# Optimization experiments

Hardware: AMD Instinct MI355X
Metric: run time of the kernel (lower is better)

## Reference

```python
import jax, jax.numpy as jnp
import numpy as np

B, F, U = 32768, 32, 256


def setup_inputs() -> dict:
    key = jax.random.key(0)
    k1, k2, k3 = jax.random.split(key, 3)
    inputs = jax.random.normal(k1, (B, F), dtype=jnp.float32)
    # weight sampled near 1 so the F-way product stays finite in fp32
    weight = 1.0 + 0.1 * jax.random.normal(k2, (F, U), dtype=jnp.float32)
    weight_selector = jax.random.normal(k3, (F, U), dtype=jnp.float32)
    bias = jnp.zeros((U,), dtype=jnp.float32)
    return {"inputs": inputs, "weight": weight,
            "weight_selector": weight_selector, "bias": bias}


def reference(inputs, weight, weight_selector, bias):
    # Faithful to CustomNeuron.call: the tf.map_fn(custom_function, ...) result
    # is dead code (immediately overwritten), so the output is
    #   prod_f( inputs[b,f] * weight[f,u] ) + bias[u]   -> [B, U]
    expand_matrix = inputs[:, :, None] * weight[None, :, :]  # [B, F, U]
    return jnp.prod(expand_matrix, axis=1) + bias  # [B, U]
```

## Files before the change

kernel.cpp:

```cpp
#include <hip/hip_runtime.h>


#define F 32
#define U 256
#define ROWS_PER_BLOCK 32

__global__ __launch_bounds__(256)
void custom_neuron_kernel(const float* __restrict__ inp,
                          const float* __restrict__ weight,
                          const float* __restrict__ bias,
                          float* __restrict__ out) {
  __shared__ float pin_s[ROWS_PER_BLOCK];
  const int tid = threadIdx.x;
  const int base = blockIdx.x * ROWS_PER_BLOCK;

  const int c = (tid & 63) * 4;
  float4 w = make_float4(1.f, 1.f, 1.f, 1.f);
#pragma unroll
  for (int f = 0; f < F; ++f) {
    const float4 wf = *(const float4*)(weight + f * U + c);
    w.x *= wf.x; w.y *= wf.y; w.z *= wf.z; w.w *= wf.w;
  }
  const float4 b = *(const float4*)(bias + c);

  {
    const float4 x = *(const float4*)(inp + (size_t)base * F + tid * 4);
    float p = x.x * x.y * x.z * x.w;
    p *= __shfl_xor(p, 1);
    p *= __shfl_xor(p, 2);
    p *= __shfl_xor(p, 4);
    if ((tid & 7) == 0) pin_s[tid >> 3] = p;
  }
  __syncthreads();

  const int r0 = tid >> 6;
#pragma unroll
  for (int k = 0; k < 8; ++k) {
    const int row = r0 + 4 * k;
    const float p = pin_s[row];
    float4 o;
    o.x = p * w.x + b.x;
    o.y = p * w.y + b.y;
    o.z = p * w.z + b.z;
    o.w = p * w.w + b.w;
    *(float4*)(out + (size_t)(base + row) * U + c) = o;
  }
}

extern "C" void kernel_launch(void* const* d_in, const int* in_sizes, int n_in,
                              void* d_out, int out_size, void* d_ws, size_t ws_size,
                              hipStream_t stream) {
  const float* inp    = (const float*)d_in[0];
  const float* weight = (const float*)d_in[1];
  const float* bias   = (const float*)d_in[3];
  float* out = (float*)d_out;

  const int B = in_sizes[0] / F;
  const int grid = B / ROWS_PER_BLOCK;
  custom_neuron_kernel<<<grid, 256, 0, stream>>>(inp, weight, bias, out);
}
```

Before: 74.67 us.

## Precompute weight column products in a separate kernel and use one row per wave

New measurement: 75.58 us. No clear change (+1.2%).

```diff
diff --git a/kernel.cpp b/kernel.cpp
--- a/kernel.cpp
+++ b/kernel.cpp
@@ -3,48 +3,44 @@
 
 #define F 32
 #define U 256
-#define ROWS_PER_BLOCK 32
+#define B_TOTAL 32768
 
 __global__ __launch_bounds__(256)
-void custom_neuron_kernel(const float* __restrict__ inp,
-                          const float* __restrict__ weight,
-                          const float* __restrict__ bias,
-                          float* __restrict__ out) {
-  __shared__ float pin_s[ROWS_PER_BLOCK];
-  const int tid = threadIdx.x;
-  const int base = blockIdx.x * ROWS_PER_BLOCK;
+void pw_kernel(const float* __restrict__ weight, float* __restrict__ pw) {
+  const int u = threadIdx.x;
+  float p = 1.0f;
+#pragma unroll
+  for (int f = 0; f < F; ++f) p *= weight[f * U + u];
+  pw[u] = p;
+}
 
-  const int c = (tid & 63) * 4;
-  float4 w = make_float4(1.f, 1.f, 1.f, 1.f);
-#pragma unroll
-  for (int f = 0; f < F; ++f) {
-    const float4 wf = *(const float4*)(weight + f * U + c);
-    w.x *= wf.x; w.y *= wf.y; w.z *= wf.z; w.w *= wf.w;
+__global__ __launch_bounds__(256)
+void main_kernel(const float* __restrict__ inp, const float* __restrict__ pw,
+                 const float* __restrict__ bias, float* __restrict__ out) {
+  const int lane = threadIdx.x & 63;
+  const int wave = threadIdx.x >> 6;
+  const int row = blockIdx.x * 4 + wave;
+
+  float p = 1.0f;
+  if (lane < 8) {
+    const float4 x = *(const float4*)(inp + (size_t)row * F + lane * 4);
+    p = x.x * x.y * x.z * x.w;
   }
-  const float4 b = *(const float4*)(bias + c);
+  p *= __shfl_xor(p, 1);
+  p *= __shfl_xor(p, 2);
+  p *= __shfl_xor(p, 4);
+  p *= __shfl_xor(p, 8);
+  p *= __shfl_xor(p, 16);
+  p *= __shfl_xor(p, 32);
 
-  {
-    const float4 x = *(const float4*)(inp + (size_t)base * F + tid * 4);
-    float p = x.x * x.y * x.z * x.w;
-    p *= __shfl_xor(p, 1);
-    p *= __shfl_xor(p, 2);
-    p *= __shfl_xor(p, 4);
-    if ((tid & 7) == 0) pin_s[tid >> 3] = p;
-  }
-  __syncthreads();
-
-  const int r0 = tid >> 6;
-#pragma unroll
-  for (int k = 0; k < 8; ++k) {
-    const int row = r0 + 4 * k;
-    const float p = pin_s[row];
-    float4 o;
-    o.x = p * w.x + b.x;
-    o.y = p * w.y + b.y;
-    o.z = p * w.z + b.z;
-    o.w = p * w.w + b.w;
-    *(float4*)(out + (size_t)(base + row) * U + c) = o;
-  }
+  const float4 w4 = *(const float4*)(pw + lane * 4);
+  const float4 b4 = *(const float4*)(bias + lane * 4);
+  float4 o;
+  o.x = p * w4.x + b4.x;
+  o.y = p * w4.y + b4.y;
+  o.z = p * w4.z + b4.z;
+  o.w = p * w4.w + b4.w;
+  *(float4*)(out + (size_t)row * U + lane * 4) = o;
 }
 
 extern "C" void kernel_launch(void* const* d_in, const int* in_sizes, int n_in,
@@ -54,8 +50,8 @@
   const float* weight = (const float*)d_in[1];
   const float* bias   = (const float*)d_in[3];
   float* out = (float*)d_out;
+  float* pw  = (float*)d_ws;
 
-  const int B = in_sizes[0] / F;
-  const int grid = B / ROWS_PER_BLOCK;
-  custom_neuron_kernel<<<grid, 256, 0, stream>>>(inp, weight, bias, out);
+  pw_kernel<<<1, 256, 0, stream>>>(weight, pw);
+  main_kernel<<<B_TOTAL / 4, 256, 0, stream>>>(inp, pw, bias, out);
 }
```
